# Kernel optimization log

Hardware: AMD Instinct MI355X
Metric: run time of the kernel (lower is better)

## Reference

```python
import jax, jax.numpy as jnp
import numpy as np

EPS = 1e-15  # matches torch_geometric GMMConv


def setup_inputs() -> dict:
    key = jax.random.key(0)
    ks = jax.random.split(key, 8)
    N, E, C_in, C_out, K, D = 163842, 1146894, 32, 32, 6, 3
    x = jax.random.normal(ks[0], (N, C_in), dtype=jnp.float32)
    edge_index = jax.random.randint(ks[1], (2, E), 0, N, dtype=jnp.int64)
    pseudo = jax.random.uniform(ks[2], (E, D), dtype=jnp.float32)
    g = jax.random.normal(ks[3], (C_in, K * C_out), dtype=jnp.float32) / np.sqrt(C_in)
    mu = jax.random.normal(ks[4], (K, D), dtype=jnp.float32)
    sigma = jax.random.uniform(ks[5], (K, D), dtype=jnp.float32) + 0.5
    root = jax.random.normal(ks[6], (C_in, C_out), dtype=jnp.float32) / np.sqrt(C_in)
    bias = jnp.zeros((C_out,), dtype=jnp.float32)
    return {"x": x, "edge_index": edge_index, "pseudo": pseudo, "g": g,
            "mu": mu, "sigma": sigma, "root": root, "bias": bias}


def reference(x, edge_index, pseudo, g, mu, sigma, root, bias):
    N = x.shape[0]
    K, D = mu.shape
    C_out = g.shape[1] // K
    src, dst = edge_index[0], edge_index[1]
    # per-node transform then gather per edge: [N, K, C_out] -> [E, K, C_out]
    xg = (x @ g).reshape(N, K, C_out)
    # Gaussian mixture weights on edge pseudo-coordinates: [E, K]
    diff = pseudo[:, None, :] - mu[None, :, :]              # [E, K, D]
    gauss = jnp.exp(jnp.sum(-0.5 * diff * diff / (EPS + sigma * sigma)[None], axis=-1))
    # weighted sum over kernels -> per-edge message [E, C_out]
    msg = jnp.einsum('eko,ek->eo', xg[src], gauss)
    # mean aggregation at destination nodes
    agg = jax.ops.segment_sum(msg, dst, num_segments=N)
    cnt = jax.ops.segment_sum(jnp.ones((src.shape[0],), x.dtype), dst, num_segments=N)
    out = agg / jnp.maximum(cnt, 1.0)[:, None]
    # root weight and bias (PyG defaults root_weight=True, bias=True)
    return out + x @ root + bias
```

## Files before the change

kernel.cpp:

```cpp
#include <hip/hip_runtime.h>
#include <hip/hip_bf16.h>

#define KD 6
#define DD 3
#define CO 32
#define CI 32
#define KC (KD * CO)
#define QP (KC / 2)

__device__ __forceinline__ uint pack_bf16(float a, float b) {
    uint lo = (uint)__bfloat16_as_ushort(__float2bfloat16(a));
    uint hi = (uint)__bfloat16_as_ushort(__float2bfloat16(b));
    return lo | (hi << 16);
}
__device__ __forceinline__ float bf_lo(uint u) { return __uint_as_float(u << 16); }
__device__ __forceinline__ float bf_hi(uint u) { return __uint_as_float(u & 0xffff0000u); }

__global__ void gauss_kernel(const float* __restrict__ pseudo, const float* __restrict__ mu,
                             const float* __restrict__ sigma, uint4* __restrict__ W, int E) {
    float m[KD][DD], iv[KD][DD];
#pragma unroll
    for (int k = 0; k < KD; ++k)
#pragma unroll
        for (int d = 0; d < DD; ++d) {
            m[k][d] = mu[k * DD + d];
            float s = sigma[k * DD + d];
            iv[k][d] = -0.5f / (1e-15f + s * s);
        }
    for (int e = blockIdx.x * blockDim.x + threadIdx.x; e < E;
         e += gridDim.x * blockDim.x) {
        float p0 = pseudo[3 * e], p1 = pseudo[3 * e + 1], p2 = pseudo[3 * e + 2];
        float w[KD];
#pragma unroll
        for (int k = 0; k < KD; ++k) {
            float d0 = p0 - m[k][0], d1 = p1 - m[k][1], d2 = p2 - m[k][2];
            w[k] = __expf(d0 * d0 * iv[k][0] + d1 * d1 * iv[k][1] + d2 * d2 * iv[k][2]);
        }
        W[e] = make_uint4(pack_bf16(w[0], w[1]), pack_bf16(w[2], w[3]),
                          pack_bf16(w[4], w[5]), 0u);
    }
}

__global__ __launch_bounds__(256, 4)
void xg_kernel(const float* __restrict__ x, const float* __restrict__ g,
               uint* __restrict__ xg, int N) {
    __shared__ float gs[CI * KC];
    for (int i = threadIdx.x; i < CI * KC; i += blockDim.x) gs[i] = g[i];
    __syncthreads();
    const int NP = (N + 1) >> 1;
    const int total = NP * 48;
    for (int idx = blockIdx.x * blockDim.x + threadIdx.x; idx < total;
         idx += gridDim.x * blockDim.x) {
        const int rp = idx / 48;
        const int t = idx - rp * 48;
        const int n0 = rp * 2;
        const int n1 = (n0 + 1 < N) ? (n0 + 1) : n0;
        const float* xr0 = x + (size_t)n0 * CI;
        const float* xr1 = x + (size_t)n1 * CI;
        float a00 = 0.f, a01 = 0.f, a02 = 0.f, a03 = 0.f;
        float a10 = 0.f, a11 = 0.f, a12 = 0.f, a13 = 0.f;
#pragma unroll 2
        for (int c = 0; c < CI; c += 4) {
            const float4 xv0 = *(const float4*)&xr0[c];
            const float4 xv1 = *(const float4*)&xr1[c];
            const float4 g0 = *(const float4*)&gs[(c + 0) * KC + 4 * t];
            const float4 g1 = *(const float4*)&gs[(c + 1) * KC + 4 * t];
            const float4 g2 = *(const float4*)&gs[(c + 2) * KC + 4 * t];
            const float4 g3 = *(const float4*)&gs[(c + 3) * KC + 4 * t];
            a00 = fmaf(xv0.x, g0.x, a00); a01 = fmaf(xv0.x, g0.y, a01);
            a02 = fmaf(xv0.x, g0.z, a02); a03 = fmaf(xv0.x, g0.w, a03);
            a10 = fmaf(xv1.x, g0.x, a10); a11 = fmaf(xv1.x, g0.y, a11);
            a12 = fmaf(xv1.x, g0.z, a12); a13 = fmaf(xv1.x, g0.w, a13);
            a00 = fmaf(xv0.y, g1.x, a00); a01 = fmaf(xv0.y, g1.y, a01);
            a02 = fmaf(xv0.y, g1.z, a02); a03 = fmaf(xv0.y, g1.w, a03);
            a10 = fmaf(xv1.y, g1.x, a10); a11 = fmaf(xv1.y, g1.y, a11);
            a12 = fmaf(xv1.y, g1.z, a12); a13 = fmaf(xv1.y, g1.w, a13);
            a00 = fmaf(xv0.z, g2.x, a00); a01 = fmaf(xv0.z, g2.y, a01);
            a02 = fmaf(xv0.z, g2.z, a02); a03 = fmaf(xv0.z, g2.w, a03);
            a10 = fmaf(xv1.z, g2.x, a10); a11 = fmaf(xv1.z, g2.y, a11);
            a12 = fmaf(xv1.z, g2.z, a12); a13 = fmaf(xv1.z, g2.w, a13);
            a00 = fmaf(xv0.w, g3.x, a00); a01 = fmaf(xv0.w, g3.y, a01);
            a02 = fmaf(xv0.w, g3.z, a02); a03 = fmaf(xv0.w, g3.w, a03);
            a10 = fmaf(xv1.w, g3.x, a10); a11 = fmaf(xv1.w, g3.y, a11);
            a12 = fmaf(xv1.w, g3.z, a12); a13 = fmaf(xv1.w, g3.w, a13);
        }
        uint2 pk0 = make_uint2(pack_bf16(a00, a01), pack_bf16(a02, a03));
        *(uint2*)(xg + (size_t)n0 * QP + 2 * t) = pk0;
        if (n0 + 1 < N) {
            uint2 pk1 = make_uint2(pack_bf16(a10, a11), pack_bf16(a12, a13));
            *(uint2*)(xg + (size_t)(n0 + 1) * QP + 2 * t) = pk1;
        }
    }
}

__global__ void edge_kernel(const int* __restrict__ ei, const uint4* __restrict__ W,
                            const uint* __restrict__ xg,
                            float* __restrict__ agg, float* __restrict__ cnt, int E) {
    const int l = threadIdx.x & 31;
    const int kbase = l >> 4;
    const int p = l & 15;
    const int gpb = blockDim.x >> 5;
    const int e0 = blockIdx.x * gpb + (threadIdx.x >> 5);
    const int estride = gridDim.x * gpb;
    for (int e = e0; e < E; e += estride) {
        const int src = ei[e];
        const int dst = ei[E + e];
        const uint4 wv = W[e];
        float wa = __uint_as_float((kbase ? (wv.x >> 16) : (wv.x & 0xffffu)) << 16);
        float wb = __uint_as_float((kbase ? (wv.y >> 16) : (wv.y & 0xffffu)) << 16);
        float wc = __uint_as_float((kbase ? (wv.z >> 16) : (wv.z & 0xffffu)) << 16);
        const uint* xr = xg + (size_t)src * QP;
        const uint u0 = xr[l];
        const uint u1 = xr[l + 32];
        const uint u2 = xr[l + 64];
        float s0 = wa * bf_lo(u0), s1 = wa * bf_hi(u0);
        s0 = fmaf(wb, bf_lo(u1), s0); s1 = fmaf(wb, bf_hi(u1), s1);
        s0 = fmaf(wc, bf_lo(u2), s0); s1 = fmaf(wc, bf_hi(u2), s1);
        s0 += __shfl_xor(s0, 16);
        s1 += __shfl_xor(s1, 16);
        const float val = kbase ? s1 : s0;
        const int ch = 2 * p + kbase;
        atomicAdd(&agg[(size_t)dst * CO + ch], val);
        if (l == 0) atomicAdd(&cnt[dst], 1.0f);
    }
}

__global__ void out_kernel(const float* __restrict__ x, const float* __restrict__ root,
                           const float* __restrict__ bias, const float* __restrict__ cnt,
                           float* __restrict__ out, int N) {
    __shared__ float rs[CI * CO];
    __shared__ float bs[CO];
    for (int i = threadIdx.x; i < CI * CO; i += blockDim.x) rs[i] = root[i];
    if (threadIdx.x < CO) bs[threadIdx.x] = bias[threadIdx.x];
    __syncthreads();
    const int total = N * 8;
    for (int idx = blockIdx.x * blockDim.x + threadIdx.x; idx < total;
         idx += gridDim.x * blockDim.x) {
        const int n = idx >> 3;
        const int t = idx & 7;
        const float* xr = x + (size_t)n * CI;
        float a0 = 0.f, a1 = 0.f, a2 = 0.f, a3 = 0.f;
#pragma unroll
        for (int c = 0; c < CI; ++c) {
            const float4 rv = *(const float4*)&rs[c * CO + 4 * t];
            float xc = xr[c];
            a0 = fmaf(xc, rv.x, a0);
            a1 = fmaf(xc, rv.y, a1);
            a2 = fmaf(xc, rv.z, a2);
            a3 = fmaf(xc, rv.w, a3);
        }
        const float inv = 1.0f / fmaxf(cnt[n], 1.0f);
        float4 o = *(float4*)&out[(size_t)n * CO + 4 * t];
        const float4 bv = *(const float4*)&bs[4 * t];
        o.x = o.x * inv + a0 + bv.x;
        o.y = o.y * inv + a1 + bv.y;
        o.z = o.z * inv + a2 + bv.z;
        o.w = o.w * inv + a3 + bv.w;
        *(float4*)&out[(size_t)n * CO + 4 * t] = o;
    }
}

extern "C" void kernel_launch(void* const* d_in, const int* in_sizes, int n_in,
                              void* d_out, int out_size, void* d_ws, size_t ws_size,
                              hipStream_t stream) {
    const float* x      = (const float*)d_in[0];
    const int*   ei     = (const int*)d_in[1];
    const float* pseudo = (const float*)d_in[2];
    const float* g      = (const float*)d_in[3];
    const float* mu     = (const float*)d_in[4];
    const float* sigma  = (const float*)d_in[5];
    const float* root   = (const float*)d_in[6];
    const float* bias   = (const float*)d_in[7];
    float* out = (float*)d_out;

    const int N = in_sizes[0] / CI;
    const int E = in_sizes[1] / 2;

    uint*  xg = (uint*)d_ws;
    uint4* W  = (uint4*)(xg + (size_t)N * QP);
    float* cnt = (float*)(W + E);

    hipMemsetAsync(d_out, 0, (size_t)out_size * sizeof(float), stream);
    hipMemsetAsync(cnt, 0, (size_t)N * sizeof(float), stream);

    const int blk = 256;

    gauss_kernel<<<(E + blk - 1) / blk, blk, 0, stream>>>(pseudo, mu, sigma, W, E);

    xg_kernel<<<2048, blk, 0, stream>>>(x, g, xg, N);

    const int gpb = blk / 32;
    int grid2 = (E + gpb - 1) / gpb;
    if (grid2 > 16384) grid2 = 16384;
    edge_kernel<<<grid2, blk, 0, stream>>>(ei, W, xg, out, cnt, E);

    int grid3 = (N * 8 + blk - 1) / blk;
    if (grid3 > 4096) grid3 = 4096;
    out_kernel<<<grid3, blk, 0, stream>>>(x, root, bias, cnt, out, N);
}
```

Baseline: 355.1 us.

## Replace atomic edge scatter with CSR counting-sort and per-node gather aggregation

Builds a CSR grouping of edges by destination: a histogram pass, a three-kernel prefix scan and a scatter that writes packed (src, bf16 gaussian weights) records. Each destination node is then aggregated by one 32-lane group without float atomics, and the mean division is folded into that kernel. This removes per-edge float atomicAdds into the output, the count array and the output memset. In exchange it adds several extra launches, an int atomic histogram and a cursor atomic per edge, and the order of summation within a node is no longer fixed.

```diff
diff --git a/kernel.cpp b/kernel.cpp
--- a/kernel.cpp
+++ b/kernel.cpp
@@ -7,6 +7,8 @@
 #define CI 32
 #define KC (KD * CO)
 #define QP (KC / 2)
+#define SCAN_T 256
+#define SCAN_B 2048
 
 __device__ __forceinline__ uint pack_bf16(float a, float b) {
     uint lo = (uint)__bfloat16_as_ushort(__float2bfloat16(a));
@@ -15,31 +17,6 @@
 }
 __device__ __forceinline__ float bf_lo(uint u) { return __uint_as_float(u << 16); }
 __device__ __forceinline__ float bf_hi(uint u) { return __uint_as_float(u & 0xffff0000u); }
-
-__global__ void gauss_kernel(const float* __restrict__ pseudo, const float* __restrict__ mu,
-                             const float* __restrict__ sigma, uint4* __restrict__ W, int E) {
-    float m[KD][DD], iv[KD][DD];
-#pragma unroll
-    for (int k = 0; k < KD; ++k)
-#pragma unroll
-        for (int d = 0; d < DD; ++d) {
-            m[k][d] = mu[k * DD + d];
-            float s = sigma[k * DD + d];
-            iv[k][d] = -0.5f / (1e-15f + s * s);
-        }
-    for (int e = blockIdx.x * blockDim.x + threadIdx.x; e < E;
-         e += gridDim.x * blockDim.x) {
-        float p0 = pseudo[3 * e], p1 = pseudo[3 * e + 1], p2 = pseudo[3 * e + 2];
-        float w[KD];
-#pragma unroll
-        for (int k = 0; k < KD; ++k) {
-            float d0 = p0 - m[k][0], d1 = p1 - m[k][1], d2 = p2 - m[k][2];
-            w[k] = __expf(d0 * d0 * iv[k][0] + d1 * d1 * iv[k][1] + d2 * d2 * iv[k][2]);
-        }
-        W[e] = make_uint4(pack_bf16(w[0], w[1]), pack_bf16(w[2], w[3]),
-                          pack_bf16(w[4], w[5]), 0u);
-    }
-}
 
 __global__ __launch_bounds__(256, 4)
 void xg_kernel(const float* __restrict__ x, const float* __restrict__ g,
@@ -93,41 +70,121 @@
     }
 }
 
-__global__ void edge_kernel(const int* __restrict__ ei, const uint4* __restrict__ W,
-                            const uint* __restrict__ xg,
-                            float* __restrict__ agg, float* __restrict__ cnt, int E) {
+__global__ void hist_kernel(const int* __restrict__ ei, int* __restrict__ hist, int E) {
+    for (int e = blockIdx.x * blockDim.x + threadIdx.x; e < E;
+         e += gridDim.x * blockDim.x)
+        atomicAdd(&hist[ei[E + e]], 1);
+}
+
+__global__ void scanA_kernel(const int* __restrict__ hist, int* __restrict__ incl,
+                             int* __restrict__ sums, int N) {
+    __shared__ int lds[SCAN_T];
+    const int t = threadIdx.x;
+    const int base = blockIdx.x * SCAN_B + t * 8;
+    int v[8]; int ts = 0;
+#pragma unroll
+    for (int j = 0; j < 8; ++j) { v[j] = (base + j < N) ? hist[base + j] : 0; ts += v[j]; }
+    lds[t] = ts; __syncthreads();
+    int acc = ts;
+    for (int off = 1; off < SCAN_T; off <<= 1) {
+        int add = (t >= off) ? lds[t - off] : 0;
+        __syncthreads();
+        acc += add; lds[t] = acc;
+        __syncthreads();
+    }
+    int run = acc - ts;
+#pragma unroll
+    for (int j = 0; j < 8; ++j) { run += v[j]; if (base + j < N) incl[base + j] = run; }
+    if (t == SCAN_T - 1) sums[blockIdx.x] = acc;
+}
+
+__global__ void scanB_kernel(int* __restrict__ sums, int nb) {
+    __shared__ int lds[SCAN_T];
+    const int t = threadIdx.x;
+    int v = (t < nb) ? sums[t] : 0;
+    lds[t] = v; __syncthreads();
+    int acc = v;
+    for (int off = 1; off < SCAN_T; off <<= 1) {
+        int add = (t >= off) ? lds[t - off] : 0;
+        __syncthreads();
+        acc += add; lds[t] = acc;
+        __syncthreads();
+    }
+    if (t < nb) sums[t] = acc - v;
+}
+
+__global__ void scanC_kernel(const int* __restrict__ incl, const int* __restrict__ sums,
+                             const int* __restrict__ hist, int* __restrict__ row_start,
+                             int* __restrict__ cursor, int N) {
+    const int i = blockIdx.x * blockDim.x + threadIdx.x;
+    if (i == 0) row_start[0] = 0;
+    if (i < N) {
+        const int fin = incl[i] + sums[i / SCAN_B];
+        row_start[i + 1] = fin;
+        cursor[i] = fin - hist[i];
+    }
+}
+
+__global__ void scatter_kernel(const int* __restrict__ ei, const float* __restrict__ pseudo,
+                               const float* __restrict__ mu, const float* __restrict__ sigma,
+                               int* __restrict__ cursor, uint4* __restrict__ sorted, int E) {
+    float m[KD][DD], iv[KD][DD];
+#pragma unroll
+    for (int k = 0; k < KD; ++k)
+#pragma unroll
+        for (int d = 0; d < DD; ++d) {
+            m[k][d] = mu[k * DD + d];
+            float s = sigma[k * DD + d];
+            iv[k][d] = -0.5f / (1e-15f + s * s);
+        }
+    for (int e = blockIdx.x * blockDim.x + threadIdx.x; e < E;
+         e += gridDim.x * blockDim.x) {
+        const int src = ei[e];
+        const int dst = ei[E + e];
+        const float p0 = pseudo[3 * e], p1 = pseudo[3 * e + 1], p2 = pseudo[3 * e + 2];
+        float w[KD];
+#pragma unroll
+        for (int k = 0; k < KD; ++k) {
+            float d0 = p0 - m[k][0], d1 = p1 - m[k][1], d2 = p2 - m[k][2];
+            w[k] = __expf(d0 * d0 * iv[k][0] + d1 * d1 * iv[k][1] + d2 * d2 * iv[k][2]);
+        }
+        const int pos = atomicAdd(&cursor[dst], 1);
+        sorted[pos] = make_uint4((uint)src, pack_bf16(w[0], w[1]),
+                                 pack_bf16(w[2], w[3]), pack_bf16(w[4], w[5]));
+    }
+}
+
+__global__ void agg_kernel(const uint4* __restrict__ sorted, const uint* __restrict__ xg,
+                           const int* __restrict__ row_start, float* __restrict__ out, int N) {
     const int l = threadIdx.x & 31;
     const int kbase = l >> 4;
     const int p = l & 15;
-    const int gpb = blockDim.x >> 5;
-    const int e0 = blockIdx.x * gpb + (threadIdx.x >> 5);
-    const int estride = gridDim.x * gpb;
-    for (int e = e0; e < E; e += estride) {
-        const int src = ei[e];
-        const int dst = ei[E + e];
-        const uint4 wv = W[e];
-        float wa = __uint_as_float((kbase ? (wv.x >> 16) : (wv.x & 0xffffu)) << 16);
-        float wb = __uint_as_float((kbase ? (wv.y >> 16) : (wv.y & 0xffffu)) << 16);
-        float wc = __uint_as_float((kbase ? (wv.z >> 16) : (wv.z & 0xffffu)) << 16);
-        const uint* xr = xg + (size_t)src * QP;
+    const int d = (blockIdx.x * blockDim.x + threadIdx.x) >> 5;
+    if (d >= N) return;
+    const int s = row_start[d];
+    const int t = row_start[d + 1];
+    float s0 = 0.f, s1 = 0.f;
+    for (int i = s; i < t; ++i) {
+        const uint4 rec = sorted[i];
+        const float wa = __uint_as_float((kbase ? (rec.y >> 16) : (rec.y & 0xffffu)) << 16);
+        const float wb = __uint_as_float((kbase ? (rec.z >> 16) : (rec.z & 0xffffu)) << 16);
+        const float wc = __uint_as_float((kbase ? (rec.w >> 16) : (rec.w & 0xffffu)) << 16);
+        const uint* xr = xg + (size_t)rec.x * QP;
         const uint u0 = xr[l];
         const uint u1 = xr[l + 32];
         const uint u2 = xr[l + 64];
-        float s0 = wa * bf_lo(u0), s1 = wa * bf_hi(u0);
+        s0 = fmaf(wa, bf_lo(u0), s0); s1 = fmaf(wa, bf_hi(u0), s1);
         s0 = fmaf(wb, bf_lo(u1), s0); s1 = fmaf(wb, bf_hi(u1), s1);
         s0 = fmaf(wc, bf_lo(u2), s0); s1 = fmaf(wc, bf_hi(u2), s1);
-        s0 += __shfl_xor(s0, 16);
-        s1 += __shfl_xor(s1, 16);
-        const float val = kbase ? s1 : s0;
-        const int ch = 2 * p + kbase;
-        atomicAdd(&agg[(size_t)dst * CO + ch], val);
-        if (l == 0) atomicAdd(&cnt[dst], 1.0f);
-    }
+    }
+    s0 += __shfl_xor(s0, 16);
+    s1 += __shfl_xor(s1, 16);
+    const float inv = 1.0f / fmaxf((float)(t - s), 1.0f);
+    out[(size_t)d * CO + 2 * p + kbase] = (kbase ? s1 : s0) * inv;
 }
 
 __global__ void out_kernel(const float* __restrict__ x, const float* __restrict__ root,
-                           const float* __restrict__ bias, const float* __restrict__ cnt,
-                           float* __restrict__ out, int N) {
+                           const float* __restrict__ bias, float* __restrict__ out, int N) {
     __shared__ float rs[CI * CO];
     __shared__ float bs[CO];
     for (int i = threadIdx.x; i < CI * CO; i += blockDim.x) rs[i] = root[i];
@@ -149,13 +206,12 @@
             a2 = fmaf(xc, rv.z, a2);
             a3 = fmaf(xc, rv.w, a3);
         }
-        const float inv = 1.0f / fmaxf(cnt[n], 1.0f);
         float4 o = *(float4*)&out[(size_t)n * CO + 4 * t];
         const float4 bv = *(const float4*)&bs[4 * t];
-        o.x = o.x * inv + a0 + bv.x;
-        o.y = o.y * inv + a1 + bv.y;
-        o.z = o.z * inv + a2 + bv.z;
-        o.w = o.w * inv + a3 + bv.w;
+        o.x = o.x + a0 + bv.x;
+        o.y = o.y + a1 + bv.y;
+        o.z = o.z + a2 + bv.z;
+        o.w = o.w + a3 + bv.w;
         *(float4*)&out[(size_t)n * CO + 4 * t] = o;
     }
 }
@@ -176,25 +232,33 @@
     const int N = in_sizes[0] / CI;
     const int E = in_sizes[1] / 2;
 
-    uint*  xg = (uint*)d_ws;
-    uint4* W  = (uint4*)(xg + (size_t)N * QP);
-    float* cnt = (float*)(W + E);
-
-    hipMemsetAsync(d_out, 0, (size_t)out_size * sizeof(float), stream);
-    hipMemsetAsync(cnt, 0, (size_t)N * sizeof(float), stream);
+    uint* xg       = (uint*)d_ws;
+    int*  hist     = (int*)(xg + (size_t)N * QP);
+    int*  incl     = hist + N;
+    int*  row_start= incl + N;
+    int*  cursor   = row_start + N + 1;
+    int*  sums     = cursor + N;
+    uint4* sorted  = (uint4*)(((uintptr_t)(sums + SCAN_T) + 15) & ~(uintptr_t)15);
+
+    hipMemsetAsync(hist, 0, (size_t)N * sizeof(int), stream);
 
     const int blk = 256;
 
-    gauss_kernel<<<(E + blk - 1) / blk, blk, 0, stream>>>(pseudo, mu, sigma, W, E);
-
     xg_kernel<<<2048, blk, 0, stream>>>(x, g, xg, N);
 
-    const int gpb = blk / 32;
-    int grid2 = (E + gpb - 1) / gpb;
-    if (grid2 > 16384) grid2 = 16384;
-    edge_kernel<<<grid2, blk, 0, stream>>>(ei, W, xg, out, cnt, E);
+    hist_kernel<<<2048, blk, 0, stream>>>(ei, hist, E);
+
+    const int nb = (N + SCAN_B - 1) / SCAN_B;
+    scanA_kernel<<<nb, SCAN_T, 0, stream>>>(hist, incl, sums, N);
+    scanB_kernel<<<1, SCAN_T, 0, stream>>>(sums, nb);
+    scanC_kernel<<<(N + blk - 1) / blk, blk, 0, stream>>>(incl, sums, hist, row_start,
+                                                         cursor, N);
+
+    scatter_kernel<<<2048, blk, 0, stream>>>(ei, pseudo, mu, sigma, cursor, sorted, E);
+
+    agg_kernel<<<(N * 32 + blk - 1) / blk, blk, 0, stream>>>(sorted, xg, row_start, out, N);
 
     int grid3 = (N * 8 + blk - 1) / blk;
     if (grid3 > 4096) grid3 = 4096;
-    out_kernel<<<grid3, blk, 0, stream>>>(x, root, bias, cnt, out, N);
-}
+    out_kernel<<<grid3, blk, 0, stream>>>(x, root, bias, out, N);
+}
```

New measurement: 375.6 us. 5.8% more time.
